# Kernel tuning notes

Hardware: AMD Instinct MI355X
Metric: run time of the kernel (lower is better)

Reference implementation:

```python
import jax, jax.numpy as jnp
import numpy as np

DIM = 512
HEAD_DIM = 32
HEADS = DIM // HEAD_DIM
WS = 7              # window_size
DISP = WS // 2      # cyclic shift displacement
SHIFTED = True


def _rel_indices(ws):
    # torch indexes pos_embedding with raw (possibly negative) distances;
    # negative python indices wrap modulo the dim size (2*ws-1).
    idx = np.array([[x, y] for x in range(ws) for y in range(ws)])
    d = idx[None, :, :] - idx[:, None, :]          # (ws^2, ws^2, 2)
    return np.mod(d, 2 * ws - 1)


def _mask(ws, disp, upper_lower, left_right):
    m = np.zeros((ws, ws, ws, ws), np.float32)
    if upper_lower:
        m[:-disp, :, -disp:, :] = -np.inf
        m[-disp:, :, :-disp, :] = -np.inf
    if left_right:
        m[:, -disp:, :, :-disp] = -np.inf
        m[:, :-disp, :, -disp:] = -np.inf
    return m.reshape(ws * ws, ws * ws)


def setup_inputs() -> dict:
    key = jax.random.key(0)
    ks = jax.random.split(key, 5)
    B, H, W = 32, 56, 56
    x = jax.random.normal(ks[0], (B, H, W, DIM), jnp.float32)
    w_qkv = jax.random.normal(ks[1], (DIM, 3 * DIM), jnp.float32) * 0.02
    pos_emb = jax.random.normal(ks[2], (2 * WS - 1, 2 * WS - 1, HEADS), jnp.float32)
    w_out = jax.random.normal(ks[3], (DIM, DIM), jnp.float32) * 0.02
    b_out = jax.random.normal(ks[4], (DIM,), jnp.float32) * 0.02
    return {"x": x, "w_qkv": w_qkv, "pos_emb": pos_emb, "w_out": w_out, "b_out": b_out}


def reference(x, w_qkv, pos_emb, w_out, b_out):
    rel = _rel_indices(WS)                         # static int constants
    ul_mask = jnp.asarray(_mask(WS, DISP, True, False))
    lr_mask = jnp.asarray(_mask(WS, DISP, False, True))

    B, H, W, _ = x.shape
    nw_h, nw_w = H // WS, W // WS

    if SHIFTED:
        x = jnp.roll(x, (-DISP, -DISP), axis=(1, 2))

    qkv = x @ w_qkv                                # (B,H,W,3*dim)

    def to_windows(t):
        # (B,H,W,dim) -> (B, heads, nw_h*nw_w, ws*ws, head_dim)
        t = t.reshape(B, nw_h, WS, nw_w, WS, HEADS, HEAD_DIM)
        return t.transpose(0, 5, 1, 3, 2, 4, 6).reshape(B, HEADS, nw_h * nw_w, WS * WS, HEAD_DIM)

    q, k, v = (to_windows(t) for t in jnp.split(qkv, 3, axis=-1))

    dots = jnp.einsum('bhwid,bhwjd->bhwij', q, k) * (HEAD_DIM ** -0.5)
    bias = pos_emb[rel[:, :, 0], rel[:, :, 1], :]  # (ws^2, ws^2, heads)
    dots = dots + bias.transpose(2, 0, 1)[None, :, None]

    if SHIFTED:
        dots = dots.at[:, :, -nw_w:].add(ul_mask)
        dots = dots.at[:, :, nw_w - 1::nw_w].add(lr_mask)

    attn = jax.nn.softmax(dots, axis=-1)
    out = jnp.einsum('bhwij,bhwjd->bhwid', attn, v)

    # (B,heads,nw,ws^2,d) -> (B,H,W,dim)
    out = out.reshape(B, HEADS, nw_h, nw_w, WS, WS, HEAD_DIM)
    out = out.transpose(0, 2, 4, 3, 5, 1, 6).reshape(B, H, W, DIM)
    out = out @ w_out + b_out

    if SHIFTED:
        out = jnp.roll(out, (DISP, DISP), axis=(1, 2))
    return out
```

## Files before the change

kernel.cpp:

```cpp
#include <hip/hip_runtime.h>
#include <hip/hip_bf16.h>
#include <stdint.h>


#define NWIN 64
#define NTOK 49
#define WIN_ELEMS 1568
#define HEAD_STRIDE 100352
#define BATCH_STRIDE 1605632
#define QKV_ELEMS 51380224
#define NTOKENS 100352
#define SCALE 0.17677669529663687f

typedef __attribute__((ext_vector_type(8))) short bf16x8;
typedef __attribute__((ext_vector_type(4))) float f32x4;

#define AS1 __attribute__((address_space(1)))
#define AS3 __attribute__((address_space(3)))

struct __align__(16) bf8 { __hip_bfloat16 h[8]; };

__device__ __forceinline__ void gload_lds16(const void* g, void* l) {
  __builtin_amdgcn_global_load_lds((const AS1 unsigned int*)g,
                                   (AS3 unsigned int*)l, 16, 0, 0);
}

__device__ __forceinline__ void token_decode(int t, int& b, int& i, int& j) {
  b = t / 3136;
  int r = t - b * 3136;
  i = r / 56;
  j = r - i * 56;
}

__global__ __launch_bounds__(256) void k_prep_lut(int* __restrict__ lutw,
                                                  int* __restrict__ luto) {
  int t = blockIdx.x * 256 + threadIdx.x;
  int b, i, j;
  token_decode(t, b, i, j);
  int win = (i / 7) * 8 + (j / 7);
  int pos = (i % 7) * 7 + (j % 7);
  lutw[t] = b * BATCH_STRIDE + win * WIN_ELEMS + pos * 32;
  int di = i + 3; if (di >= 56) di -= 56;
  int dj = j + 3; if (dj >= 56) dj -= 56;
  luto[t] = ((b * 56 + di) * 56 + dj) * 512;
}

__global__ __launch_bounds__(256) void k_prep_x(const float* __restrict__ x,
                                                __hip_bfloat16* __restrict__ xb) {
  int idx = blockIdx.x * 256 + threadIdx.x;
  int t = idx >> 6;
  int c = (idx & 63) * 8;
  int b, i, j;
  token_decode(t, b, i, j);
  int si = i + 3; if (si >= 56) si -= 56;
  int sj = j + 3; if (sj >= 56) sj -= 56;
  const float* src = x + ((size_t)(b * 56 + si) * 56 + sj) * 512 + c;
  float4 a0 = *(const float4*)src;
  float4 a1 = *(const float4*)(src + 4);
  bf8 o;
  o.h[0] = __float2bfloat16(a0.x); o.h[1] = __float2bfloat16(a0.y);
  o.h[2] = __float2bfloat16(a0.z); o.h[3] = __float2bfloat16(a0.w);
  o.h[4] = __float2bfloat16(a1.x); o.h[5] = __float2bfloat16(a1.y);
  o.h[6] = __float2bfloat16(a1.z); o.h[7] = __float2bfloat16(a1.w);
  *(bf8*)(xb + (size_t)t * 512 + c) = o;
}

__global__ __launch_bounds__(256) void k_transpose(const float* __restrict__ in,
                                                   __hip_bfloat16* __restrict__ out,
                                                   int K, int N) {
  __shared__ float tl[64][65];
  const int nb = blockIdx.x * 64, kb = blockIdx.y * 64;
  const int tid = threadIdx.x;
#pragma unroll
  for (int s = 0; s < 16; ++s) {
    int idx = s * 256 + tid; int r = idx >> 6, c = idx & 63;
    tl[r][c] = in[(size_t)(kb + r) * N + nb + c];
  }
  __syncthreads();
#pragma unroll
  for (int s = 0; s < 16; ++s) {
    int idx = s * 256 + tid; int r = idx >> 6, c = idx & 63;
    out[(size_t)(nb + r) * K + kb + c] = __float2bfloat16(tl[c][r]);
  }
}

__global__ __launch_bounds__(256) void k_prep_bias(const float* __restrict__ pe,
                                                   float* __restrict__ biasT) {
  int id = blockIdx.x * 256 + threadIdx.x;
  int whid = id >> 12;
  int wtype = whid >> 4, h = whid & 15;
  int mid = id & 4095;
  int mf = mid >> 10, r = (mid >> 8) & 3, lane = (mid >> 2) & 63, nf = mid & 3;
  int key = mf * 16 + (lane >> 4) * 4 + r;
  int query = nf * 16 + (lane & 15);
  float v;
  if (key >= 49 || query >= 49) {
    v = -1e30f;
  } else {
    int i = query, j = key;
    int xi = i / 7, yi = i - xi * 7;
    int xj = j / 7, yj = j - xj * 7;
    int dx = xj - xi; if (dx < 0) dx += 13;
    int dy = yj - yi; if (dy < 0) dy += 13;
    v = pe[(dx * 13 + dy) * 16 + h];
    if ((wtype & 1) && ((xi >= 4) != (xj >= 4))) v = -1e30f;
    if ((wtype & 2) && ((yi >= 4) != (yj >= 4))) v = -1e30f;
  }
  biasT[id] = v;
}

__global__ __launch_bounds__(256) void k_qkv_mfma(
    const __hip_bfloat16* __restrict__ xb, const __hip_bfloat16* __restrict__ wbt,
    const int* __restrict__ lutw,
    __hip_bfloat16* __restrict__ qb, __hip_bfloat16* __restrict__ kb,
    __hip_bfloat16* __restrict__ vb) {
  __shared__ __align__(16) short As[128 * 64];
  __shared__ __align__(16) short Bs[128 * 64];
  const int tid = threadIdx.x;
  const int lid = blockIdx.x;
  const int wid = (lid & 7) * 1176 + (lid >> 3);
  const int t0 = (wid / 12) * 128;
  const int n0 = (wid % 12) * 128;
  const int lane = tid & 63, wave = tid >> 6;
  const int wm = wave >> 1, wn = wave & 1;

  const __hip_bfloat16* asrc[4];
  const __hip_bfloat16* bsrc[4];
#pragma unroll
  for (int s = 0; s < 4; ++s) {
    int c = s * 256 + tid;
    int row = c >> 3, kc = c & 7;
    asrc[s] = xb + (size_t)(t0 + row) * 512 + kc * 8;
    bsrc[s] = wbt + (size_t)(n0 + row) * 512 + kc * 8;
  }
  char* abase = (char*)As + wave * 1024;
  char* bbase = (char*)Bs + wave * 1024;

  f32x4 acc[4][4] = {};
  const int arow = wm * 64 + (lane & 15);
  const int brow = wn * 64 + (lane & 15);
  const int koff = (lane >> 4) * 8;

  for (int kt = 0; kt < 512; kt += 64) {
#pragma unroll
    for (int s = 0; s < 4; ++s) gload_lds16(asrc[s] + kt, abase + s * 4096);
#pragma unroll
    for (int s = 0; s < 4; ++s) gload_lds16(bsrc[s] + kt, bbase + s * 4096);
    __syncthreads();
    bf16x8 af[2][4], bfr[2][4];
#pragma unroll
    for (int kk = 0; kk < 2; ++kk) {
#pragma unroll
      for (int mf = 0; mf < 4; ++mf)
        af[kk][mf] = *(const bf16x8*)&As[(arow + mf * 16) * 64 + kk * 32 + koff];
#pragma unroll
      for (int nf = 0; nf < 4; ++nf)
        bfr[kk][nf] = *(const bf16x8*)&Bs[(brow + nf * 16) * 64 + kk * 32 + koff];
    }
#pragma unroll
    for (int kk = 0; kk < 2; ++kk)
#pragma unroll
      for (int mf = 0; mf < 4; ++mf)
#pragma unroll
        for (int nf = 0; nf < 4; ++nf)
          acc[mf][nf] = __builtin_amdgcn_mfma_f32_16x16x32_bf16(
              af[kk][mf], bfr[kk][nf], acc[mf][nf], 0, 0, 0);
    __syncthreads();
  }

  __hip_bfloat16* obs[4];
#pragma unroll
  for (int nf = 0; nf < 4; ++nf) {
    int n = n0 + wn * 64 + nf * 16 + (lane & 15);
    int sp = n >> 9, hc = n & 511, h = hc >> 5, d = hc & 31;
    obs[nf] = (sp == 0 ? qb : (sp == 1 ? kb : vb)) + (size_t)h * HEAD_STRIDE + d;
  }
  const int tbase = t0 + wm * 64 + (lane >> 4) * 4;
  int woff[4][4];
#pragma unroll
  for (int mf = 0; mf < 4; ++mf)
#pragma unroll
    for (int r = 0; r < 4; ++r)
      woff[mf][r] = lutw[tbase + mf * 16 + r];
#pragma unroll
  for (int mf = 0; mf < 4; ++mf)
#pragma unroll
    for (int r = 0; r < 4; ++r) {
      size_t off = (size_t)woff[mf][r];
#pragma unroll
      for (int nf = 0; nf < 4; ++nf)
        obs[nf][off] = __float2bfloat16(acc[mf][nf][r]);
    }
}

__global__ __launch_bounds__(256) void k_attn_mfma(
    const __hip_bfloat16* __restrict__ qb, const __hip_bfloat16* __restrict__ kb,
    const __hip_bfloat16* __restrict__ vb, const float* __restrict__ biasT,
    __hip_bfloat16* __restrict__ ab) {
  __shared__ __align__(16) __hip_bfloat16 P[4][64 * 72];
  __shared__ __align__(16) __hip_bfloat16 VT[4][32 * 64];
  const int tid = threadIdx.x, lane = tid & 63, wave = tid >> 6;
  const int gid = blockIdx.x * 4 + wave;
  const int win = gid & 63, h = (gid >> 6) & 15;
  const int wtype = (((win >> 3) == 7) ? 1 : 0) | (((win & 7) == 7) ? 2 : 0);
  const size_t qkbase = (size_t)gid * WIN_ELEMS;
  const int fr = lane & 15, fo = (lane >> 4) * 8;

  bf8 v8[4];
#pragma unroll
  for (int it = 0; it < 4; ++it) {
    int c = it * 64 + lane;
    if (c < 196) v8[it] = *(const bf8*)(vb + qkbase + (size_t)c * 8);
  }

  bf16x8 kf[4], qf[4];
#pragma unroll
  for (int f = 0; f < 4; ++f) {
    kf[f] = *(const bf16x8*)(kb + qkbase + (size_t)(f * 16 + fr) * 32 + fo);
    qf[f] = *(const bf16x8*)(qb + qkbase + (size_t)(f * 16 + fr) * 32 + fo);
  }

  __hip_bfloat16* vtw = VT[wave];
  {
    bf16x8 zz = {};
#pragma unroll
    for (int z = 0; z < 4; ++z) *(bf16x8*)&vtw[z * 512 + lane * 8] = zz;
  }
#pragma unroll
  for (int it = 0; it < 4; ++it) {
    int c = it * 64 + lane;
    if (c < 196) {
      int pos = c >> 2, d0 = (c & 3) * 8;
#pragma unroll
      for (int u = 0; u < 8; ++u) {
        int d = d0 + u;
        vtw[d * 64 + (pos ^ ((d & 7) << 3))] = v8[it].h[u];
      }
    }
  }

  f32x4 sacc[4][4] = {};
#pragma unroll
  for (int mf = 0; mf < 4; ++mf)
#pragma unroll
    for (int nf = 0; nf < 4; ++nf)
      sacc[mf][nf] = __builtin_amdgcn_mfma_f32_16x16x32_bf16(
          kf[mf], qf[nf], sacc[mf][nf], 0, 0, 0);

  const float* bp = biasT + (size_t)(wtype * 16 + h) * 4096;
#pragma unroll
  for (int mf = 0; mf < 4; ++mf)
#pragma unroll
    for (int r = 0; r < 4; ++r) {
      float4 bv = *(const float4*)(bp + ((mf * 4 + r) * 64 + lane) * 4);
      sacc[mf][0][r] = fmaf(sacc[mf][0][r], SCALE, bv.x);
      sacc[mf][1][r] = fmaf(sacc[mf][1][r], SCALE, bv.y);
      sacc[mf][2][r] = fmaf(sacc[mf][2][r], SCALE, bv.z);
      sacc[mf][3][r] = fmaf(sacc[mf][3][r], SCALE, bv.w);
    }

  float inv[4];
#pragma unroll
  for (int nf = 0; nf < 4; ++nf) {
    float m = sacc[0][nf][0];
#pragma unroll
    for (int mf = 0; mf < 4; ++mf)
#pragma unroll
      for (int r = 0; r < 4; ++r) m = fmaxf(m, sacc[mf][nf][r]);
    m = fmaxf(m, __shfl_xor(m, 16));
    m = fmaxf(m, __shfl_xor(m, 32));
    float sum = 0.f;
#pragma unroll
    for (int mf = 0; mf < 4; ++mf)
#pragma unroll
      for (int r = 0; r < 4; ++r) {
        float e = __expf(sacc[mf][nf][r] - m);
        sacc[mf][nf][r] = e;
        sum += e;
      }
    sum += __shfl_xor(sum, 16);
    sum += __shfl_xor(sum, 32);
    inv[nf] = 1.0f / sum;
  }

  __hip_bfloat16* pw = P[wave];
#pragma unroll
  for (int mf = 0; mf < 4; ++mf)
#pragma unroll
    for (int r = 0; r < 4; ++r) {
      int key = mf * 16 + (lane >> 4) * 4 + r;
#pragma unroll
      for (int nf = 0; nf < 4; ++nf) {
        int query = nf * 16 + fr;
        pw[query * 72 + key] = __float2bfloat16(sacc[mf][nf][r] * inv[nf]);
      }
    }

  f32x4 oacc[4][2] = {};
#pragma unroll
  for (int kk = 0; kk < 2; ++kk) {
    bf16x8 vf[2];
#pragma unroll
    for (int n2 = 0; n2 < 2; ++n2) {
      int d = n2 * 16 + fr;
      vf[n2] = *(const bf16x8*)&vtw[d * 64 + ((kk * 32 + fo) ^ ((d & 7) << 3))];
    }
#pragma unroll
    for (int mf = 0; mf < 4; ++mf) {
      bf16x8 pa = *(const bf16x8*)&pw[(mf * 16 + fr) * 72 + kk * 32 + fo];
#pragma unroll
      for (int n2 = 0; n2 < 2; ++n2)
        oacc[mf][n2] = __builtin_amdgcn_mfma_f32_16x16x32_bf16(
            pa, vf[n2], oacc[mf][n2], 0, 0, 0);
    }
  }

#pragma unroll
  for (int mf = 0; mf < 4; ++mf)
#pragma unroll
    for (int r = 0; r < 4; ++r) {
      int row = mf * 16 + (lane >> 4) * 4 + r;
      if (row < 49) {
#pragma unroll
        for (int n2 = 0; n2 < 2; ++n2)
          ab[qkbase + (size_t)row * 32 + n2 * 16 + fr] =
              __float2bfloat16(oacc[mf][n2][r]);
      }
    }
}

__global__ __launch_bounds__(256) void k_out_mfma(
    const __hip_bfloat16* __restrict__ ab, const __hip_bfloat16* __restrict__ wot,
    const int* __restrict__ lutw, const int* __restrict__ luto,
    const float* __restrict__ bias, float* __restrict__ out) {
  __shared__ __align__(16) short As[128 * 64];
  __shared__ __align__(16) short Bs[128 * 64];
  const int tid = threadIdx.x;
  const int lid = blockIdx.x;
  const int wid = (lid & 7) * 392 + (lid >> 3);
  const int t0 = (wid >> 2) * 128;
  const int n0 = (wid & 3) * 128;
  const int lane = tid & 63, wave = tid >> 6;
  const int wm = wave >> 1, wn = wave & 1;

  size_t aoff[4];
  const __hip_bfloat16* bsrc[4];
#pragma unroll
  for (int s = 0; s < 4; ++s) {
    int c = s * 256 + tid;
    int row = c >> 3, kc = c & 7;
    aoff[s] = (size_t)lutw[t0 + row] + (size_t)(kc >> 2) * HEAD_STRIDE + (kc & 3) * 8;
    bsrc[s] = wot + (size_t)(n0 + row) * 512 + kc * 8;
  }
  char* abase = (char*)As + wave * 1024;
  char* bbase = (char*)Bs + wave * 1024;

  f32x4 acc[4][4] = {};
  const int arow = wm * 64 + (lane & 15);
  const int brow = wn * 64 + (lane & 15);
  const int koff = (lane >> 4) * 8;

  for (int kt = 0; kt < 512; kt += 64) {
    size_t hoff = (size_t)(kt >> 5) * HEAD_STRIDE;
#pragma unroll
    for (int s = 0; s < 4; ++s) gload_lds16(ab + aoff[s] + hoff, abase + s * 4096);
#pragma unroll
    for (int s = 0; s < 4; ++s) gload_lds16(bsrc[s] + kt, bbase + s * 4096);
    __syncthreads();
    bf16x8 af[2][4], bfr[2][4];
#pragma unroll
    for (int kk = 0; kk < 2; ++kk) {
#pragma unroll
      for (int mf = 0; mf < 4; ++mf)
        af[kk][mf] = *(const bf16x8*)&As[(arow + mf * 16) * 64 + kk * 32 + koff];
#pragma unroll
      for (int nf = 0; nf < 4; ++nf)
        bfr[kk][nf] = *(const bf16x8*)&Bs[(brow + nf * 16) * 64 + kk * 32 + koff];
    }
#pragma unroll
    for (int kk = 0; kk < 2; ++kk)
#pragma unroll
      for (int mf = 0; mf < 4; ++mf)
#pragma unroll
        for (int nf = 0; nf < 4; ++nf)
          acc[mf][nf] = __builtin_amdgcn_mfma_f32_16x16x32_bf16(
              af[kk][mf], bfr[kk][nf], acc[mf][nf], 0, 0, 0);
    __syncthreads();
  }

  float bia[4];
#pragma unroll
  for (int nf = 0; nf < 4; ++nf)
    bia[nf] = bias[n0 + wn * 64 + nf * 16 + (lane & 15)];

  const int tbase = t0 + wm * 64 + (lane >> 4) * 4;
  int ooff[4][4];
#pragma unroll
  for (int mf = 0; mf < 4; ++mf)
#pragma unroll
    for (int r = 0; r < 4; ++r)
      ooff[mf][r] = luto[tbase + mf * 16 + r];
#pragma unroll
  for (int mf = 0; mf < 4; ++mf) {
#pragma unroll
    for (int r = 0; r < 4; ++r) {
      float* op = out + (size_t)ooff[mf][r] + n0 + wn * 64 + (lane & 15);
#pragma unroll
      for (int nf = 0; nf < 4; ++nf) op[nf * 16] = acc[mf][nf][r] + bia[nf];
    }
  }
}

extern "C" void kernel_launch(void* const* d_in, const int* in_sizes, int n_in,
                              void* d_out, int out_size, void* d_ws, size_t ws_size,
                              hipStream_t stream) {
  const float* x     = (const float*)d_in[0];
  const float* w_qkv = (const float*)d_in[1];
  const float* pe    = (const float*)d_in[2];
  const float* w_out = (const float*)d_in[3];
  const float* b_out = (const float*)d_in[4];
  float* out = (float*)d_out;

  __hip_bfloat16* qb  = (__hip_bfloat16*)d_ws;
  __hip_bfloat16* kb  = qb + (size_t)QKV_ELEMS;
  __hip_bfloat16* vb  = kb + (size_t)QKV_ELEMS;
  __hip_bfloat16* xb  = vb + (size_t)QKV_ELEMS;
  __hip_bfloat16* ab  = xb;
  __hip_bfloat16* wbt = xb + (size_t)QKV_ELEMS;
  __hip_bfloat16* wot = wbt + (size_t)(1536 * 512);
  float* biasT = (float*)(wot + (size_t)(512 * 512));
  int* lutw = (int*)(biasT + 262144);
  int* luto = lutw + NTOKENS;

  k_prep_lut<<<dim3(392), dim3(256), 0, stream>>>(lutw, luto);
  k_prep_x<<<dim3(25088), dim3(256), 0, stream>>>(x, xb);
  k_transpose<<<dim3(24, 8), dim3(256), 0, stream>>>(w_qkv, wbt, 512, 1536);
  k_transpose<<<dim3(8, 8), dim3(256), 0, stream>>>(w_out, wot, 512, 512);
  k_prep_bias<<<dim3(1024), dim3(256), 0, stream>>>(pe, biasT);
  k_qkv_mfma<<<dim3(9408), dim3(256), 0, stream>>>(xb, wbt, lutw, qb, kb, vb);
  k_attn_mfma<<<dim3(8192), dim3(256), 0, stream>>>(qb, kb, vb, biasT, ab);
  k_out_mfma<<<dim3(3136), dim3(256), 0, stream>>>(ab, wot, lutw, luto, b_out, out);
}
```

Baseline: 588.9 us.

## Fuse fp32 input cast and shift into QKV GEMM, double-buffer both GEMMs

Removes the separate rolled fp32-to-bf16 conversion pass of x. The QKV GEMM now reads fp32 x through a shift lookup table, converts it in registers and writes bf16 into LDS. Both the QKV and output-projection GEMMs gain double-buffered LDS, prefetching the next k-tile while the current one is computed. This saves a full write and read of the bf16 activation buffer, but it doubles LDS use per block, which can lower occupancy, and each QKV tile block (12 per token tile) now reads fp32 x, double the bytes of the old bf16 copy.

Result: slower. 738.5 us (+25.4%).

```diff
diff --git a/kernel.cpp b/kernel.cpp
--- a/kernel.cpp
+++ b/kernel.cpp
@@ -32,37 +32,30 @@
   j = r - i * 56;
 }
 
-__global__ __launch_bounds__(256) void k_prep_lut(int* __restrict__ lutw,
+__device__ __forceinline__ bf8 pack8(const float4& a, const float4& b) {
+  bf8 o;
+  o.h[0] = __float2bfloat16(a.x); o.h[1] = __float2bfloat16(a.y);
+  o.h[2] = __float2bfloat16(a.z); o.h[3] = __float2bfloat16(a.w);
+  o.h[4] = __float2bfloat16(b.x); o.h[5] = __float2bfloat16(b.y);
+  o.h[6] = __float2bfloat16(b.z); o.h[7] = __float2bfloat16(b.w);
+  return o;
+}
+
+__global__ __launch_bounds__(256) void k_prep_lut(int* __restrict__ lutr,
+                                                  int* __restrict__ lutw,
                                                   int* __restrict__ luto) {
   int t = blockIdx.x * 256 + threadIdx.x;
   int b, i, j;
   token_decode(t, b, i, j);
+  int si = i + 3; if (si >= 56) si -= 56;
+  int sj = j + 3; if (sj >= 56) sj -= 56;
+  lutr[t] = ((b * 56 + si) * 56 + sj) * 512;
   int win = (i / 7) * 8 + (j / 7);
   int pos = (i % 7) * 7 + (j % 7);
   lutw[t] = b * BATCH_STRIDE + win * WIN_ELEMS + pos * 32;
   int di = i + 3; if (di >= 56) di -= 56;
   int dj = j + 3; if (dj >= 56) dj -= 56;
   luto[t] = ((b * 56 + di) * 56 + dj) * 512;
-}
-
-__global__ __launch_bounds__(256) void k_prep_x(const float* __restrict__ x,
-                                                __hip_bfloat16* __restrict__ xb) {
-  int idx = blockIdx.x * 256 + threadIdx.x;
-  int t = idx >> 6;
-  int c = (idx & 63) * 8;
-  int b, i, j;
-  token_decode(t, b, i, j);
-  int si = i + 3; if (si >= 56) si -= 56;
-  int sj = j + 3; if (sj >= 56) sj -= 56;
-  const float* src = x + ((size_t)(b * 56 + si) * 56 + sj) * 512 + c;
-  float4 a0 = *(const float4*)src;
-  float4 a1 = *(const float4*)(src + 4);
-  bf8 o;
-  o.h[0] = __float2bfloat16(a0.x); o.h[1] = __float2bfloat16(a0.y);
-  o.h[2] = __float2bfloat16(a0.z); o.h[3] = __float2bfloat16(a0.w);
-  o.h[4] = __float2bfloat16(a1.x); o.h[5] = __float2bfloat16(a1.y);
-  o.h[6] = __float2bfloat16(a1.z); o.h[7] = __float2bfloat16(a1.w);
-  *(bf8*)(xb + (size_t)t * 512 + c) = o;
 }
 
 __global__ __launch_bounds__(256) void k_transpose(const float* __restrict__ in,
@@ -110,12 +103,12 @@
 }
 
 __global__ __launch_bounds__(256) void k_qkv_mfma(
-    const __hip_bfloat16* __restrict__ xb, const __hip_bfloat16* __restrict__ wbt,
-    const int* __restrict__ lutw,
+    const float* __restrict__ x, const __hip_bfloat16* __restrict__ wbt,
+    const int* __restrict__ lutr, const int* __restrict__ lutw,
     __hip_bfloat16* __restrict__ qb, __hip_bfloat16* __restrict__ kb,
     __hip_bfloat16* __restrict__ vb) {
-  __shared__ __align__(16) short As[128 * 64];
-  __shared__ __align__(16) short Bs[128 * 64];
+  __shared__ __align__(16) short As[2][128 * 64];
+  __shared__ __align__(16) short Bs[2][128 * 64];
   const int tid = threadIdx.x;
   const int lid = blockIdx.x;
   const int wid = (lid & 7) * 1176 + (lid >> 3);
@@ -124,38 +117,57 @@
   const int lane = tid & 63, wave = tid >> 6;
   const int wm = wave >> 1, wn = wave & 1;
 
-  const __hip_bfloat16* asrc[4];
+  const int arow_s = tid >> 1, aseg = tid & 1;
+  const float* axp = x + (size_t)lutr[t0 + arow_s] + aseg * 32;
+  short* adst = &As[0][arow_s * 64 + aseg * 32];
+
   const __hip_bfloat16* bsrc[4];
 #pragma unroll
   for (int s = 0; s < 4; ++s) {
     int c = s * 256 + tid;
     int row = c >> 3, kc = c & 7;
-    asrc[s] = xb + (size_t)(t0 + row) * 512 + kc * 8;
     bsrc[s] = wbt + (size_t)(n0 + row) * 512 + kc * 8;
   }
-  char* abase = (char*)As + wave * 1024;
-  char* bbase = (char*)Bs + wave * 1024;
 
   f32x4 acc[4][4] = {};
   const int arow = wm * 64 + (lane & 15);
   const int brow = wn * 64 + (lane & 15);
   const int koff = (lane >> 4) * 8;
 
+  float4 ar[8];
+#pragma unroll
+  for (int u = 0; u < 8; ++u) ar[u] = ((const float4*)axp)[u];
+#pragma unroll
+  for (int s = 0; s < 4; ++s)
+    gload_lds16(bsrc[s], (char*)Bs[0] + wave * 1024 + s * 4096);
+#pragma unroll
+  for (int v = 0; v < 4; ++v)
+    *(bf8*)(adst + v * 8) = pack8(ar[2 * v], ar[2 * v + 1]);
+  __syncthreads();
+
+  int buf = 0;
   for (int kt = 0; kt < 512; kt += 64) {
-#pragma unroll
-    for (int s = 0; s < 4; ++s) gload_lds16(asrc[s] + kt, abase + s * 4096);
-#pragma unroll
-    for (int s = 0; s < 4; ++s) gload_lds16(bsrc[s] + kt, bbase + s * 4096);
-    __syncthreads();
+    const bool pf = (kt < 448);
+    if (pf) {
+      const float* p = axp + kt + 64;
+#pragma unroll
+      for (int u = 0; u < 8; ++u) ar[u] = ((const float4*)p)[u];
+#pragma unroll
+      for (int s = 0; s < 4; ++s)
+        gload_lds16(bsrc[s] + kt + 64,
+                    (char*)Bs[buf ^ 1] + wave * 1024 + s * 4096);
+    }
+    const short* Ab = As[buf];
+    const short* Bb = Bs[buf];
     bf16x8 af[2][4], bfr[2][4];
 #pragma unroll
     for (int kk = 0; kk < 2; ++kk) {
 #pragma unroll
       for (int mf = 0; mf < 4; ++mf)
-        af[kk][mf] = *(const bf16x8*)&As[(arow + mf * 16) * 64 + kk * 32 + koff];
+        af[kk][mf] = *(const bf16x8*)&Ab[(arow + mf * 16) * 64 + kk * 32 + koff];
 #pragma unroll
       for (int nf = 0; nf < 4; ++nf)
-        bfr[kk][nf] = *(const bf16x8*)&Bs[(brow + nf * 16) * 64 + kk * 32 + koff];
+        bfr[kk][nf] = *(const bf16x8*)&Bb[(brow + nf * 16) * 64 + kk * 32 + koff];
     }
 #pragma unroll
     for (int kk = 0; kk < 2; ++kk)
@@ -165,7 +177,14 @@
         for (int nf = 0; nf < 4; ++nf)
           acc[mf][nf] = __builtin_amdgcn_mfma_f32_16x16x32_bf16(
               af[kk][mf], bfr[kk][nf], acc[mf][nf], 0, 0, 0);
+    if (pf) {
+      short* ad = adst + (buf ^ 1) * 8192;
+#pragma unroll
+      for (int v = 0; v < 4; ++v)
+        *(bf8*)(ad + v * 8) = pack8(ar[2 * v], ar[2 * v + 1]);
+    }
     __syncthreads();
+    buf ^= 1;
   }
 
   __hip_bfloat16* obs[4];
@@ -333,8 +352,8 @@
     const __hip_bfloat16* __restrict__ ab, const __hip_bfloat16* __restrict__ wot,
     const int* __restrict__ lutw, const int* __restrict__ luto,
     const float* __restrict__ bias, float* __restrict__ out) {
-  __shared__ __align__(16) short As[128 * 64];
-  __shared__ __align__(16) short Bs[128 * 64];
+  __shared__ __align__(16) short As[2][128 * 64];
+  __shared__ __align__(16) short Bs[2][128 * 64];
   const int tid = threadIdx.x;
   const int lid = blockIdx.x;
   const int wid = (lid & 7) * 392 + (lid >> 3);
@@ -352,30 +371,40 @@
     aoff[s] = (size_t)lutw[t0 + row] + (size_t)(kc >> 2) * HEAD_STRIDE + (kc & 3) * 8;
     bsrc[s] = wot + (size_t)(n0 + row) * 512 + kc * 8;
   }
-  char* abase = (char*)As + wave * 1024;
-  char* bbase = (char*)Bs + wave * 1024;
 
   f32x4 acc[4][4] = {};
   const int arow = wm * 64 + (lane & 15);
   const int brow = wn * 64 + (lane & 15);
   const int koff = (lane >> 4) * 8;
 
+#pragma unroll
+  for (int s = 0; s < 4; ++s) {
+    gload_lds16(ab + aoff[s], (char*)As[0] + wave * 1024 + s * 4096);
+    gload_lds16(bsrc[s], (char*)Bs[0] + wave * 1024 + s * 4096);
+  }
+  __syncthreads();
+
+  int buf = 0;
   for (int kt = 0; kt < 512; kt += 64) {
-    size_t hoff = (size_t)(kt >> 5) * HEAD_STRIDE;
-#pragma unroll
-    for (int s = 0; s < 4; ++s) gload_lds16(ab + aoff[s] + hoff, abase + s * 4096);
-#pragma unroll
-    for (int s = 0; s < 4; ++s) gload_lds16(bsrc[s] + kt, bbase + s * 4096);
-    __syncthreads();
+    if (kt < 448) {
+      size_t hoff = (size_t)((kt + 64) >> 5) * HEAD_STRIDE;
+#pragma unroll
+      for (int s = 0; s < 4; ++s) {
+        gload_lds16(ab + aoff[s] + hoff, (char*)As[buf ^ 1] + wave * 1024 + s * 4096);
+        gload_lds16(bsrc[s] + kt + 64, (char*)Bs[buf ^ 1] + wave * 1024 + s * 4096);
+      }
+    }
+    const short* Ab = As[buf];
+    const short* Bb = Bs[buf];
     bf16x8 af[2][4], bfr[2][4];
 #pragma unroll
     for (int kk = 0; kk < 2; ++kk) {
 #pragma unroll
       for (int mf = 0; mf < 4; ++mf)
-        af[kk][mf] = *(const bf16x8*)&As[(arow + mf * 16) * 64 + kk * 32 + koff];
+        af[kk][mf] = *(const bf16x8*)&Ab[(arow + mf * 16) * 64 + kk * 32 + koff];
 #pragma unroll
       for (int nf = 0; nf < 4; ++nf)
-        bfr[kk][nf] = *(const bf16x8*)&Bs[(brow + nf * 16) * 64 + kk * 32 + koff];
+        bfr[kk][nf] = *(const bf16x8*)&Bb[(brow + nf * 16) * 64 + kk * 32 + koff];
     }
 #pragma unroll
     for (int kk = 0; kk < 2; ++kk)
@@ -386,6 +415,7 @@
           acc[mf][nf] = __builtin_amdgcn_mfma_f32_16x16x32_bf16(
               af[kk][mf], bfr[kk][nf], acc[mf][nf], 0, 0, 0);
     __syncthreads();
+    buf ^= 1;
   }
 
   float bia[4];
@@ -424,20 +454,19 @@
   __hip_bfloat16* qb  = (__hip_bfloat16*)d_ws;
   __hip_bfloat16* kb  = qb + (size_t)QKV_ELEMS;
   __hip_bfloat16* vb  = kb + (size_t)QKV_ELEMS;
-  __hip_bfloat16* xb  = vb + (size_t)QKV_ELEMS;
-  __hip_bfloat16* ab  = xb;
-  __hip_bfloat16* wbt = xb + (size_t)QKV_ELEMS;
+  __hip_bfloat16* ab  = vb + (size_t)QKV_ELEMS;
+  __hip_bfloat16* wbt = ab + (size_t)QKV_ELEMS;
   __hip_bfloat16* wot = wbt + (size_t)(1536 * 512);
   float* biasT = (float*)(wot + (size_t)(512 * 512));
-  int* lutw = (int*)(biasT + 262144);
+  int* lutr = (int*)(biasT + 262144);
+  int* lutw = lutr + NTOKENS;
   int* luto = lutw + NTOKENS;
 
-  k_prep_lut<<<dim3(392), dim3(256), 0, stream>>>(lutw, luto);
-  k_prep_x<<<dim3(25088), dim3(256), 0, stream>>>(x, xb);
+  k_prep_lut<<<dim3(392), dim3(256), 0, stream>>>(lutr, lutw, luto);
   k_transpose<<<dim3(24, 8), dim3(256), 0, stream>>>(w_qkv, wbt, 512, 1536);
   k_transpose<<<dim3(8, 8), dim3(256), 0, stream>>>(w_out, wot, 512, 512);
   k_prep_bias<<<dim3(1024), dim3(256), 0, stream>>>(pe, biasT);
-  k_qkv_mfma<<<dim3(9408), dim3(256), 0, stream>>>(xb, wbt, lutw, qb, kb, vb);
+  k_qkv_mfma<<<dim3(9408), dim3(256), 0, stream>>>(x, wbt, lutr, lutw, qb, kb, vb);
   k_attn_mfma<<<dim3(8192), dim3(256), 0, stream>>>(qb, kb, vb, biasT, ab);
   k_out_mfma<<<dim3(3136), dim3(256), 0, stream>>>(ab, wot, lutw, luto, b_out, out);
 }
```
